# Kernel tuning notes

Measured on AMD Instinct MI355X. Metric: run time of the kernel, lower is better.

## Reference

```python
import jax, jax.numpy as jnp
import numpy as np


def setup_inputs() -> dict:
    key = jax.random.key(0)
    k1, k2 = jax.random.split(key)
    x = jax.random.normal(k1, (16, 1, 512, 512), dtype=jnp.float32)
    weight = jax.random.normal(k2, (128, 1), dtype=jnp.float32)
    return {"x": x, "weight": weight}


def reference(x, weight):
    # x: [B, C=1, H, W]; weight: [K=128, D=1] codebook
    inputs = jnp.transpose(x, (0, 2, 3, 1))          # [B, H, W, C]
    input_shape = inputs.shape
    D = weight.shape[1]
    flat = inputs.reshape(-1, D)                     # [N, D]
    # pairwise squared distances: ||z||^2 + ||e||^2 - 2 z.e^T  -> [N, K]
    dist = (jnp.sum(flat ** 2, axis=1, keepdims=True)
            + jnp.sum(weight ** 2, axis=1)
            - 2.0 * flat @ weight.T)
    idx = jnp.argmin(dist, axis=1)                   # [N]
    # one-hot @ weight == gather of codebook rows (same math, no [N,K] one-hot)
    quantized = weight[idx].reshape(input_shape)     # [B, H, W, C]
    return jnp.transpose(quantized, (0, 3, 1, 2))    # [B, C, H, W]
```

## Files before the change

### kernel.cpp

```cpp
#include <hip/hip_runtime.h>


constexpr int K     = 128;
constexpr int NB    = 1024;
constexpr int EPT   = 8;
constexpr int BLOCK = 256;

#define DELTA 0.0125f

__global__ __launch_bounds__(BLOCK) void vq_kernel(const float* __restrict__ x,
                                                   const float* __restrict__ w,
                                                   float* __restrict__ out,
                                                   long n, int kk) {
#pragma clang fp contract(off)
    __shared__ float wraw[K];
    __shared__ float svw[2 * K];
    __shared__ int   si[K];
    __shared__ int   lut[NB];

    const int t = threadIdx.x;
    if (t < K) {
        wraw[t]    = (t < kk) ? w[t] : __builtin_inff();
        svw[t]     = __builtin_inff();
        svw[K + t] = __builtin_inff();
        si[t]      = 0x7fffffff;
    }
    __syncthreads();
    if (t < kk) {
        float v = wraw[t];
        int rank = 0;
        for (int j = 0; j < kk; ++j) {
            float u = wraw[j];
            rank += (u < v) || (u == v && j < t);
        }
        float v2 = v * v;
        asm volatile("" : "+v"(v2));
        svw[rank]     = v;
        svw[K + rank] = v2;
        si[rank]      = t;
    }
    __syncthreads();

    const float lo    = svw[0];
    const float hi    = svw[kk - 1];
    const float range = hi - lo;
    const float scale = (range > 0.f) ? (float)NB / range : 0.f;
    const float binv  = (range > 0.f) ? range / (float)NB : 0.f;
    const int   sMax  = (kk > 8 ? kk : 8) - 8;

    for (int b = t; b < NB; b += BLOCK) {
        float L = lo + ((float)b - 1.5f) * binv;
        float R = lo + ((float)b + 2.5f) * binv;
        int pL = 0;
#pragma unroll
        for (int st = 64; st > 0; st >>= 1)
            if (svw[pL + st - 1] < L) pL += st;
        if (svw[pL] < L) ++pL;
        int pR = 0;
#pragma unroll
        for (int st = 64; st > 0; st >>= 1)
            if (svw[pR + st - 1] < R) pR += st;
        if (svw[pR] < R) ++pR;

        float wa  = svw[pL > 0 ? pL - 1 : 0];
        float wb  = svw[pR < kk ? pR : kk - 1];
        float tlo = wa - DELTA;
        float thi = wb + DELTA;

        int s0 = pL > 0 ? pL - 1 : 0;
        while (s0 > 0 && svw[s0 - 1] >= tlo) --s0;
        int e0 = pR;
        while (e0 < kk && svw[e0] <= thi) ++e0;

        if (s0 > sMax) s0 = sMax;
        lut[b] = s0 | (e0 << 8);
    }
    __syncthreads();

    long base = ((long)blockIdx.x * BLOCK + t) * (long)EPT;
    if (base + EPT <= n) {
        float4 a  = *(const float4*)(x + base);
        float4 b4 = *(const float4*)(x + base + 4);
        float xs[EPT] = {a.x, a.y, a.z, a.w, b4.x, b4.y, b4.z, b4.w};
        float res[EPT];
#pragma unroll
        for (int e = 0; e < EPT; ++e) {
            float xv = xs[e];
            float x2 = xv * xv;
            asm volatile("" : "+v"(x2));
            float tx = xv + xv;

            float fi = (xv - lo) * scale;
            int idx = (int)fi;
            idx = idx < 0 ? 0 : (idx > NB - 1 ? NB - 1 : idx);
            int pk = lut[idx];
            int s  = pk & 0xff;
            int en = pk >> 8;

            float best = __builtin_inff();
            float bw   = 0.0f;
            unsigned tie = 0u;
#pragma unroll
            for (int c = 0; c < 8; ++c) {
                float wv = svw[s + c];
                float w2 = svw[K + s + c];
                float sum  = x2 + w2;
                float prod = tx * wv;
                asm volatile("" : "+v"(prod));
                float d = sum - prod;
                bool lt = d < best;
                tie |= (d == best) ? 1u : 0u;
                best = lt ? d : best;
                bw   = lt ? wv : bw;
            }
            if (__builtin_expect(en > s + 8, 0)) {
                for (int j = s + 8; j < en; ++j) {
                    float wv = svw[j];
                    float w2 = svw[K + j];
                    float sum  = x2 + w2;
                    float prod = tx * wv;
                    asm volatile("" : "+v"(prod));
                    float d = sum - prod;
                    bool lt = d < best;
                    tie |= (d == best) ? 1u : 0u;
                    best = lt ? d : best;
                    bw   = lt ? wv : bw;
                }
            }
            res[e] = bw;
            if (__builtin_expect(tie != 0u, 0)) {
                int hiEnd = en > s + 8 ? en : s + 8;
                float bb = __builtin_inff(), bwv = 0.0f;
                int bi = 0x7fffffff;
                for (int j = s; j < hiEnd; ++j) {
                    float wv = svw[j];
                    float w2 = svw[K + j];
                    float sum  = x2 + w2;
                    float prod = tx * wv;
                    asm volatile("" : "+v"(prod));
                    float d = sum - prod;
                    int oi = si[j];
                    if (d < bb || (d == bb && oi < bi)) { bb = d; bi = oi; bwv = wv; }
                }
                res[e] = bwv;
            }
        }
        *(float4*)(out + base)     = make_float4(res[0], res[1], res[2], res[3]);
        *(float4*)(out + base + 4) = make_float4(res[4], res[5], res[6], res[7]);
    } else {
        for (long i = base; i < n; ++i) {
            float xv = x[i];
            float x2 = xv * xv;
            asm volatile("" : "+v"(x2));
            float tx = xv + xv;
            float bb = __builtin_inff(), bwv = 0.0f;
            int bi = 0x7fffffff;
            for (int p0 = 0; p0 < kk; ++p0) {
                float wv = svw[p0];
                float w2 = svw[K + p0];
                float sum  = x2 + w2;
                float prod = tx * wv;
                asm volatile("" : "+v"(prod));
                float d = sum - prod;
                int oi = si[p0];
                if (d < bb || (d == bb && oi < bi)) { bb = d; bi = oi; bwv = wv; }
            }
            out[i] = bwv;
        }
    }
}

extern "C" void kernel_launch(void* const* d_in, const int* in_sizes, int n_in,
                              void* d_out, int out_size, void* d_ws, size_t ws_size,
                              hipStream_t stream) {
    const float* x = (const float*)d_in[0];
    const float* w = (const float*)d_in[1];
    float* out     = (float*)d_out;
    long n = (long)in_sizes[0];
    int  kk = in_sizes[1] < K ? in_sizes[1] : K;

    long threads_needed = (n + EPT - 1) / EPT;
    long grid = (threads_needed + BLOCK - 1) / BLOCK;
    vq_kernel<<<(int)grid, BLOCK, 0, stream>>>(x, w, out, n, kk);
}
```

Before: 90.74 us.

## Build sorted codebook and lookup table once in a separate prologue kernel

```diff
diff --git a/kernel.cpp b/kernel.cpp
--- a/kernel.cpp
+++ b/kernel.cpp
@@ -6,24 +6,25 @@
 constexpr int EPT   = 8;
 constexpr int BLOCK = 256;
 
+constexpr int SV_OFF  = 0;
+constexpr int SI_OFF  = K;
+constexpr int LUT_OFF = 2 * K;
+constexpr int HDR_OFF = 2 * K + NB;
+
 #define DELTA 0.0125f
 
-__global__ __launch_bounds__(BLOCK) void vq_kernel(const float* __restrict__ x,
-                                                   const float* __restrict__ w,
-                                                   float* __restrict__ out,
-                                                   long n, int kk) {
+__global__ __launch_bounds__(BLOCK) void vq_build(const float* __restrict__ w,
+                                                  float* __restrict__ ws,
+                                                  int kk) {
 #pragma clang fp contract(off)
     __shared__ float wraw[K];
-    __shared__ float svw[2 * K];
-    __shared__ int   si[K];
-    __shared__ int   lut[NB];
-
+    __shared__ float sv[K];
+    __shared__ int   sidx[K];
     const int t = threadIdx.x;
     if (t < K) {
-        wraw[t]    = (t < kk) ? w[t] : __builtin_inff();
-        svw[t]     = __builtin_inff();
-        svw[K + t] = __builtin_inff();
-        si[t]      = 0x7fffffff;
+        wraw[t] = (t < kk) ? w[t] : __builtin_inff();
+        sv[t]   = __builtin_inff();
+        sidx[t] = 0x7fffffff;
     }
     __syncthreads();
     if (t < kk) {
@@ -33,48 +34,82 @@
             float u = wraw[j];
             rank += (u < v) || (u == v && j < t);
         }
-        float v2 = v * v;
-        asm volatile("" : "+v"(v2));
-        svw[rank]     = v;
-        svw[K + rank] = v2;
-        si[rank]      = t;
+        sv[rank]   = v;
+        sidx[rank] = t;
     }
     __syncthreads();
 
-    const float lo    = svw[0];
-    const float hi    = svw[kk - 1];
+    const float lo    = sv[0];
+    const float hi    = sv[kk - 1];
     const float range = hi - lo;
     const float scale = (range > 0.f) ? (float)NB / range : 0.f;
     const float binv  = (range > 0.f) ? range / (float)NB : 0.f;
     const int   sMax  = (kk > 8 ? kk : 8) - 8;
 
-    for (int b = t; b < NB; b += BLOCK) {
-        float L = lo + ((float)b - 1.5f) * binv;
-        float R = lo + ((float)b + 2.5f) * binv;
-        int pL = 0;
-#pragma unroll
-        for (int st = 64; st > 0; st >>= 1)
-            if (svw[pL + st - 1] < L) pL += st;
-        if (svw[pL] < L) ++pL;
-        int pR = 0;
-#pragma unroll
-        for (int st = 64; st > 0; st >>= 1)
-            if (svw[pR + st - 1] < R) pR += st;
-        if (svw[pR] < R) ++pR;
-
-        float wa  = svw[pL > 0 ? pL - 1 : 0];
-        float wb  = svw[pR < kk ? pR : kk - 1];
+    if (t < K) {
+        ws[SV_OFF + t] = sv[t];
+        ((int*)ws)[SI_OFF + t] = sidx[t];
+    }
+    if (t == 0) {
+        ws[HDR_OFF]     = lo;
+        ws[HDR_OFF + 1] = scale;
+    }
+
+    const int b0 = t * 4;
+    float L0 = lo + ((float)b0 - 1.5f) * binv;
+    float R0 = lo + ((float)b0 + 2.5f) * binv;
+    int pL = 0, pR = 0;
+#pragma unroll
+    for (int st = 64; st > 0; st >>= 1)
+        if (sv[pL + st - 1] < L0) pL += st;
+    if (pL < K && sv[pL] < L0) ++pL;
+#pragma unroll
+    for (int st = 64; st > 0; st >>= 1)
+        if (sv[pR + st - 1] < R0) pR += st;
+    if (pR < K && sv[pR] < R0) ++pR;
+
+    for (int j = 0; j < 4; ++j) {
+        int b = b0 + j;
+        float Lb = lo + ((float)b - 1.5f) * binv;
+        float Rb = lo + ((float)b + 2.5f) * binv;
+        while (pL < kk && sv[pL] < Lb) ++pL;
+        while (pR < kk && sv[pR] < Rb) ++pR;
+
+        float wa  = sv[pL > 0 ? pL - 1 : 0];
+        float wb  = sv[pR < kk ? pR : kk - 1];
         float tlo = wa - DELTA;
         float thi = wb + DELTA;
 
         int s0 = pL > 0 ? pL - 1 : 0;
-        while (s0 > 0 && svw[s0 - 1] >= tlo) --s0;
+        while (s0 > 0 && sv[s0 - 1] >= tlo) --s0;
         int e0 = pR;
-        while (e0 < kk && svw[e0] <= thi) ++e0;
+        while (e0 < kk && sv[e0] <= thi) ++e0;
 
         if (s0 > sMax) s0 = sMax;
-        lut[b] = s0 | (e0 << 8);
-    }
+        ((int*)ws)[LUT_OFF + b] = s0 | (e0 << 8);
+    }
+}
+
+__global__ __launch_bounds__(BLOCK) void vq_main(const float* __restrict__ x,
+                                                 const float* __restrict__ ws,
+                                                 float* __restrict__ out,
+                                                 long n, int kk) {
+#pragma clang fp contract(off)
+    __shared__ float sv[K];
+    __shared__ int   si[K];
+    __shared__ alignas(16) int lut[NB];
+
+    const int t = threadIdx.x;
+    if (t < K) {
+        sv[t] = ws[SV_OFF + t];
+        si[t] = ((const int*)ws)[SI_OFF + t];
+    }
+    {
+        int4 lv = ((const int4*)(ws + LUT_OFF))[t];
+        *(int4*)&lut[4 * t] = lv;
+    }
+    const float lo    = ws[HDR_OFF];
+    const float scale = ws[HDR_OFF + 1];
     __syncthreads();
 
     long base = ((long)blockIdx.x * BLOCK + t) * (long)EPT;
@@ -102,8 +137,9 @@
             unsigned tie = 0u;
 #pragma unroll
             for (int c = 0; c < 8; ++c) {
-                float wv = svw[s + c];
-                float w2 = svw[K + s + c];
+                float wv = sv[s + c];
+                float w2 = wv * wv;
+                asm volatile("" : "+v"(w2));
                 float sum  = x2 + w2;
                 float prod = tx * wv;
                 asm volatile("" : "+v"(prod));
@@ -115,8 +151,9 @@
             }
             if (__builtin_expect(en > s + 8, 0)) {
                 for (int j = s + 8; j < en; ++j) {
-                    float wv = svw[j];
-                    float w2 = svw[K + j];
+                    float wv = sv[j];
+                    float w2 = wv * wv;
+                    asm volatile("" : "+v"(w2));
                     float sum  = x2 + w2;
                     float prod = tx * wv;
                     asm volatile("" : "+v"(prod));
@@ -133,8 +170,9 @@
                 float bb = __builtin_inff(), bwv = 0.0f;
                 int bi = 0x7fffffff;
                 for (int j = s; j < hiEnd; ++j) {
-                    float wv = svw[j];
-                    float w2 = svw[K + j];
+                    float wv = sv[j];
+                    float w2 = wv * wv;
+                    asm volatile("" : "+v"(w2));
                     float sum  = x2 + w2;
                     float prod = tx * wv;
                     asm volatile("" : "+v"(prod));
@@ -156,8 +194,9 @@
             float bb = __builtin_inff(), bwv = 0.0f;
             int bi = 0x7fffffff;
             for (int p0 = 0; p0 < kk; ++p0) {
-                float wv = svw[p0];
-                float w2 = svw[K + p0];
+                float wv = sv[p0];
+                float w2 = wv * wv;
+                asm volatile("" : "+v"(w2));
                 float sum  = x2 + w2;
                 float prod = tx * wv;
                 asm volatile("" : "+v"(prod));
@@ -176,10 +215,13 @@
     const float* x = (const float*)d_in[0];
     const float* w = (const float*)d_in[1];
     float* out     = (float*)d_out;
+    float* ws      = (float*)d_ws;
     long n = (long)in_sizes[0];
     int  kk = in_sizes[1] < K ? in_sizes[1] : K;
 
+    vq_build<<<1, BLOCK, 0, stream>>>(w, ws, kk);
+
     long threads_needed = (n + EPT - 1) / EPT;
     long grid = (threads_needed + BLOCK - 1) / BLOCK;
-    vq_kernel<<<(int)grid, BLOCK, 0, stream>>>(x, w, out, n, kk);
+    vq_main<<<(int)grid, BLOCK, 0, stream>>>(x, ws, out, n, kk);
 }
```

Result: no change. 89.99 us (-0.8%).
